# Kernel optimization log

Hardware: AMD Instinct MI355X
Metric: run time of the kernel (lower is better)

## Reference

```python
import jax, jax.numpy as jnp
import numpy as np

HIDDEN = 2048
VOCAB = 32768
SEQ = 4608
N_CHUNKS = 9
CAP = 30.0
IGNORE = -100


def setup_inputs() -> dict:
    key = jax.random.key(0)
    k1, k2, k3 = jax.random.split(key, 3)
    weight = (jax.random.normal(k1, (VOCAB, HIDDEN), dtype=jnp.float32) * 0.02).astype(jnp.bfloat16)
    hidden = jax.random.normal(k2, (1, SEQ, HIDDEN), dtype=jnp.float32)
    input_ids = jax.random.randint(k3, (1, SEQ), 0, VOCAB)
    attention_mask = jnp.ones((1, SEQ), dtype=jnp.int32)
    return {"weight": weight, "hidden": hidden, "input_ids": input_ids,
            "attention_mask": attention_mask}


def _build_labels(input_ids, attention_mask):
    # labels[t] = input_ids[t+1], masked-out positions and the final position -> -100
    ids = input_ids[0]
    am = attention_mask[0]
    lab = jnp.where(am[1:] == 0, IGNORE, ids[1:])            # [S-1]
    lab = jnp.concatenate([lab, jnp.full((1,), IGNORE, lab.dtype)])  # [S]
    return lab


def reference(weight, hidden, input_ids, attention_mask):
    labels = _build_labels(input_ids, attention_mask)        # [S]
    x = hidden.reshape(-1, HIDDEN)                           # [S, H] fp32
    chunk = SEQ // N_CHUNKS
    xs = x.reshape(N_CHUNKS, chunk, HIDDEN)
    ls = labels.reshape(N_CHUNKS, chunk)

    wT = weight.T                                            # [H, V] bf16

    def chunk_loss(args):
        xc, lc = args                                        # [c,H], [c]
        # softcapped logits: CAP * tanh((x @ W^T) / CAP), mm in bf16
        t = jnp.tanh((xc.astype(jnp.bfloat16) @ wT) / CAP).astype(jnp.float32)  # [c,V]
        z = CAP * (t - jnp.max(t, axis=1, keepdims=True))    # stable shifted logits
        logp = z - jnp.log(jnp.sum(jnp.exp(z), axis=1, keepdims=True))
        valid = lc != IGNORE
        idx = jnp.where(valid, lc, 0)
        nll = -jnp.take_along_axis(logp, idx[:, None], axis=1)[:, 0]
        return jnp.sum(jnp.where(valid, nll, 0.0))

    losses = jax.lax.map(chunk_loss, (xs, ls))               # [N_CHUNKS]
    return jnp.sum(losses)
```

## Files before the change

### kernel.cpp

```cpp
#include <hip/hip_runtime.h>
#include <hip/hip_bf16.h>
#include <cstdint>

#define S_LEN   4608
#define HID     2048
#define VOCAB_N 32768
#define CAPV    30.0f
#define IGNORE_IDX (-100)
#define NT512   512

typedef short bf16x8 __attribute__((ext_vector_type(8)));
typedef float f32x4  __attribute__((ext_vector_type(4)));

__device__ __forceinline__ unsigned short f2bf_rtne(float f) {
    unsigned int u = __float_as_uint(f);
    unsigned int r = u + 0x7fffu + ((u >> 16) & 1u);
    return (unsigned short)(r >> 16);
}
__device__ __forceinline__ float bfr(float f) {
    unsigned int u = __float_as_uint(f);
    unsigned int r = u + 0x7fffu + ((u >> 16) & 1u);
    return __uint_as_float(r & 0xffff0000u);
}
__device__ __forceinline__ float bf_lo(unsigned int u) { return __uint_as_float(u << 16); }
__device__ __forceinline__ float bf_hi(unsigned int u) { return __uint_as_float(u & 0xffff0000u); }
__device__ __forceinline__ float bfdot2(unsigned int x, unsigned int w) {
    return bf_lo(x) * bf_lo(w) + bf_hi(x) * bf_hi(w);
}
__device__ __forceinline__ float softcap_ref(float logit) {
    float lb = bfr(logit);
    float x  = bfr(lb / CAPV);
    float e  = __expf(2.0f * x);
    float t  = bfr((e - 1.0f) / (e + 1.0f));
    return CAPV * t;
}

__global__ void cvt_kernel(const float* __restrict__ h, unsigned short* __restrict__ xb,
                           float* __restrict__ out) {
    if (blockIdx.x == 0 && threadIdx.x == 0) out[0] = 0.0f;
    int i = blockIdx.x * blockDim.x + threadIdx.x;
    float4 v = ((const float4*)h)[i];
    ushort4 o;
    o.x = f2bf_rtne(v.x); o.y = f2bf_rtne(v.y);
    o.z = f2bf_rtne(v.z); o.w = f2bf_rtne(v.w);
    ((ushort4*)xb)[i] = o;
}

__global__ void gemm_lse_kernel(const unsigned short* __restrict__ X,
                                const unsigned short* __restrict__ W,
                                float* __restrict__ partL) {
    __shared__ __align__(16) unsigned short As[128 * 32];
    __shared__ __align__(16) unsigned short Bs[128 * 32];

    const int tid  = threadIdx.x;
    const int wave = tid >> 6;
    const int lane = tid & 63;
    const int tileM = blockIdx.x * 128;
    const int tileN = blockIdx.y * 128;

    const int lr = lane >> 2;
    const int cg = (lane & 3) ^ ((lane >> 4) & 3);

    const unsigned short* Abase = X + (size_t)(tileM + wave * 32) * HID + cg * 8;
    const unsigned short* Bbase = W + (size_t)(tileN + wave * 32) * HID + cg * 8;

    const int wr  = wave >> 1, wc = wave & 1;
    const int q   = lane >> 4, l16 = lane & 15;

    const int swz = (q ^ (l16 >> 2)) * 8;
    int arow[4], brow[4];
    #pragma unroll
    for (int t = 0; t < 4; ++t) {
        arow[t] = (wr * 64 + t * 16 + l16) * 32 + swz;
        brow[t] = (wc * 64 + t * 16 + l16) * 32 + swz;
    }

    f32x4 acc[4][4] = {};

    for (int k0 = 0; k0 < HID; k0 += 32) {
        __syncthreads();
        #pragma unroll
        for (int j = 0; j < 2; ++j) {
            const unsigned short* ga = Abase + (size_t)(j * 16 + lr) * HID + k0;
            __builtin_amdgcn_global_load_lds(
                (const __attribute__((address_space(1))) void*)ga,
                (__attribute__((address_space(3))) void*)&As[(wave * 32 + j * 16) * 32],
                16, 0, 0);
            const unsigned short* gb = Bbase + (size_t)(j * 16 + lr) * HID + k0;
            __builtin_amdgcn_global_load_lds(
                (const __attribute__((address_space(1))) void*)gb,
                (__attribute__((address_space(3))) void*)&Bs[(wave * 32 + j * 16) * 32],
                16, 0, 0);
        }
        __syncthreads();

        bf16x8 av[4], bv[4];
        #pragma unroll
        for (int t = 0; t < 4; ++t) {
            av[t] = *(const bf16x8*)&As[arow[t]];
            bv[t] = *(const bf16x8*)&Bs[brow[t]];
        }
        #pragma unroll
        for (int ti = 0; ti < 4; ++ti)
            #pragma unroll
            for (int tj = 0; tj < 4; ++tj)
                acc[ti][tj] = __builtin_amdgcn_mfma_f32_16x16x32_bf16(
                    av[ti], bv[tj], acc[ti][tj], 0, 0, 0);
    }

    const int rowbase = tileM + wr * 64;
    const int ntile   = blockIdx.y * 2 + wc;
    #pragma unroll
    for (int ti = 0; ti < 4; ++ti) {
        #pragma unroll
        for (int r = 0; r < 4; ++r) {
            float s = 0.0f;
            #pragma unroll
            for (int tj = 0; tj < 4; ++tj)
                s += __expf(softcap_ref(acc[ti][tj][r]));
            s += __shfl_xor(s, 1);
            s += __shfl_xor(s, 2);
            s += __shfl_xor(s, 4);
            s += __shfl_xor(s, 8);
            if (l16 == 0)
                partL[(size_t)(rowbase + ti * 16 + q * 4 + r) * NT512 + ntile] = s;
        }
    }
}

__global__ void row_reduce_kernel(const unsigned short* __restrict__ X,
                                  const unsigned short* __restrict__ W,
                                  const int* __restrict__ ids,
                                  const int* __restrict__ am,
                                  const float* __restrict__ partL,
                                  float* __restrict__ out) {
    __shared__ float blk[4];
    const int wave = threadIdx.x >> 6;
    const int lane = threadIdx.x & 63;
    const int r = blockIdx.x * 4 + wave;

    int lab = IGNORE_IDX;
    if (r < S_LEN - 1 && am[r + 1] != 0) lab = ids[r + 1];
    const bool valid = (lab >= 0 && lab < VOCAB_N);

    float dot = 0.0f;
    if (valid) {
        const unsigned short* xr = X + (size_t)r   * HID;
        const unsigned short* wr = W + (size_t)lab * HID;
        #pragma unroll
        for (int c = 0; c < 4; ++c) {
            const int off = c * 512 + lane * 8;
            uint4 xu = *(const uint4*)(xr + off);
            uint4 wu = *(const uint4*)(wr + off);
            dot += bfdot2(xu.x, wu.x) + bfdot2(xu.y, wu.y) +
                   bfdot2(xu.z, wu.z) + bfdot2(xu.w, wu.w);
        }
    }
    #pragma unroll
    for (int m = 1; m < 64; m <<= 1) dot += __shfl_xor(dot, m);

    float L = 0.0f;
    const float* pr = partL + (size_t)r * NT512;
    #pragma unroll
    for (int i = 0; i < 8; ++i) L += pr[i * 64 + lane];
    #pragma unroll
    for (int m = 1; m < 64; m <<= 1) L += __shfl_xor(L, m);

    if (lane == 0) {
        float loss = 0.0f;
        if (valid) loss = logf(L) - softcap_ref(dot);
        blk[wave] = loss;
    }
    __syncthreads();
    if (threadIdx.x == 0)
        atomicAdd(out, blk[0] + blk[1] + blk[2] + blk[3]);
}

extern "C" void kernel_launch(void* const* d_in, const int* in_sizes, int n_in,
                              void* d_out, int out_size, void* d_ws, size_t ws_size,
                              hipStream_t stream) {
    const unsigned short* W  = (const unsigned short*)d_in[0];
    const float*  hidden     = (const float*)d_in[1];
    const int*    ids        = (const int*)d_in[2];
    const int*    am         = (const int*)d_in[3];
    float* out = (float*)d_out;

    char* ws = (char*)d_ws;
    unsigned short* Xb = (unsigned short*)ws;
    float* partL       = (float*)(ws + (size_t)S_LEN * HID * 2);

    cvt_kernel<<<(S_LEN * HID / 4) / 256, 256, 0, stream>>>(hidden, Xb, out);

    dim3 g(S_LEN / 128, VOCAB_N / 128);
    gemm_lse_kernel<<<g, 256, 0, stream>>>(Xb, W, partL);

    row_reduce_kernel<<<S_LEN / 4, 256, 0, stream>>>(Xb, W, ids, am, partL, out);
}
```

Baseline: 1.019 ms.

## Use 256x256 tiles with double-buffered LDS and interleaved load/MFMA schedule

Rewrites the GEMM+LSE kernel to use 256x256 output tiles, 512 threads (8 waves) and a 64-wide K step. Global-to-LDS copies are double-buffered and interleaved with MFMA quarters under barriers and s_setprio, so memory latency overlaps compute. The larger tile raises arithmetic intensity and cuts the number of barriers per FLOP, at the cost of 128KB of LDS, heavy register use and a complex hand-written schedule.

```diff
diff --git a/kernel.cpp b/kernel.cpp
--- a/kernel.cpp
+++ b/kernel.cpp
@@ -8,6 +8,7 @@
 #define CAPV    30.0f
 #define IGNORE_IDX (-100)
 #define NT512   512
+#define NKT     32
 
 typedef short bf16x8 __attribute__((ext_vector_type(8)));
 typedef float f32x4  __attribute__((ext_vector_type(4)));
@@ -46,86 +47,155 @@
     ((ushort4*)xb)[i] = o;
 }
 
-__global__ void gemm_lse_kernel(const unsigned short* __restrict__ X,
-                                const unsigned short* __restrict__ W,
-                                float* __restrict__ partL) {
-    __shared__ __align__(16) unsigned short As[128 * 32];
-    __shared__ __align__(16) unsigned short Bs[128 * 32];
+__global__ __launch_bounds__(512, 2)
+void gemm_lse_kernel(const unsigned short* __restrict__ X,
+                     const unsigned short* __restrict__ W,
+                     float* __restrict__ partL) {
+    __shared__ __align__(16) unsigned short As[2][256 * 64];
+    __shared__ __align__(16) unsigned short Bs[2][256 * 64];
 
     const int tid  = threadIdx.x;
-    const int wave = tid >> 6;
+    const int wid  = tid >> 6;
     const int lane = tid & 63;
-    const int tileM = blockIdx.x * 128;
-    const int tileN = blockIdx.y * 128;
-
-    const int lr = lane >> 2;
-    const int cg = (lane & 3) ^ ((lane >> 4) & 3);
-
-    const unsigned short* Abase = X + (size_t)(tileM + wave * 32) * HID + cg * 8;
-    const unsigned short* Bbase = W + (size_t)(tileN + wave * 32) * HID + cg * 8;
-
-    const int wr  = wave >> 1, wc = wave & 1;
-    const int q   = lane >> 4, l16 = lane & 15;
-
-    const int swz = (q ^ (l16 >> 2)) * 8;
-    int arow[4], brow[4];
-    #pragma unroll
-    for (int t = 0; t < 4; ++t) {
-        arow[t] = (wr * 64 + t * 16 + l16) * 32 + swz;
-        brow[t] = (wc * 64 + t * 16 + l16) * 32 + swz;
-    }
-
-    f32x4 acc[4][4] = {};
-
-    for (int k0 = 0; k0 < HID; k0 += 32) {
-        __syncthreads();
-        #pragma unroll
-        for (int j = 0; j < 2; ++j) {
-            const unsigned short* ga = Abase + (size_t)(j * 16 + lr) * HID + k0;
-            __builtin_amdgcn_global_load_lds(
-                (const __attribute__((address_space(1))) void*)ga,
-                (__attribute__((address_space(3))) void*)&As[(wave * 32 + j * 16) * 32],
-                16, 0, 0);
-            const unsigned short* gb = Bbase + (size_t)(j * 16 + lr) * HID + k0;
-            __builtin_amdgcn_global_load_lds(
-                (const __attribute__((address_space(1))) void*)gb,
-                (__attribute__((address_space(3))) void*)&Bs[(wave * 32 + j * 16) * 32],
-                16, 0, 0);
-        }
-        __syncthreads();
-
-        bf16x8 av[4], bv[4];
-        #pragma unroll
-        for (int t = 0; t < 4; ++t) {
-            av[t] = *(const bf16x8*)&As[arow[t]];
-            bv[t] = *(const bf16x8*)&Bs[brow[t]];
-        }
-        #pragma unroll
-        for (int ti = 0; ti < 4; ++ti)
-            #pragma unroll
-            for (int tj = 0; tj < 4; ++tj)
-                acc[ti][tj] = __builtin_amdgcn_mfma_f32_16x16x32_bf16(
-                    av[ti], bv[tj], acc[ti][tj], 0, 0, 0);
-    }
-
-    const int rowbase = tileM + wr * 64;
-    const int ntile   = blockIdx.y * 2 + wc;
-    #pragma unroll
-    for (int ti = 0; ti < 4; ++ti) {
+    const int wr   = wid >> 2;
+    const int wc   = wid & 3;
+    const int q    = lane >> 4, l16 = lane & 15;
+    const int tileM = blockIdx.x * 256;
+    const int tileN = blockIdx.y * 256;
+
+    const int srow = lane >> 3;
+    const int csrc = (lane & 7) ^ srow;
+    const unsigned short* Ag = X + (size_t)(tileM + wid * 8 + srow) * HID + csrc * 8;
+    const unsigned short* Wg = W + (size_t)(tileN + wid * 8 + srow) * HID + csrc * 8;
+
+    const int abase = (wr * 128 + l16) * 64;
+    const int bbase = (wc * 64  + l16) * 64;
+    const int koff0 = ((q    ) ^ (l16 & 7)) * 8;
+    const int koff1 = ((q + 4) ^ (l16 & 7)) * 8;
+
+    bf16x8 av[8][2], bv[4][2];
+    f32x4  acc[8][4] = {};
+
+#define STAGE_A(BUF, H, KT) do {                                                          \
+    const unsigned short* _g = Ag + (size_t)(H) * 128 * HID + (size_t)(KT) * 64;          \
+    __builtin_amdgcn_global_load_lds(                                                     \
+        (const __attribute__((address_space(1))) void*)_g,                                \
+        (__attribute__((address_space(3))) void*)&As[BUF][((H) * 128 + wid * 8) * 64],    \
+        16, 0, 0);                                                                        \
+    __builtin_amdgcn_global_load_lds(                                                     \
+        (const __attribute__((address_space(1))) void*)(_g + (size_t)64 * HID),           \
+        (__attribute__((address_space(3))) void*)&As[BUF][((H) * 128 + 64 + wid * 8) * 64],\
+        16, 0, 0);                                                                        \
+} while (0)
+
+#define STAGE_B(BUF, H, KT) do {                                                          \
+    const unsigned short* _g = Wg + (size_t)(H) * 128 * HID + (size_t)(KT) * 64;          \
+    __builtin_amdgcn_global_load_lds(                                                     \
+        (const __attribute__((address_space(1))) void*)_g,                                \
+        (__attribute__((address_space(3))) void*)&Bs[BUF][((H) * 128 + wid * 8) * 64],    \
+        16, 0, 0);                                                                        \
+    __builtin_amdgcn_global_load_lds(                                                     \
+        (const __attribute__((address_space(1))) void*)(_g + (size_t)64 * HID),           \
+        (__attribute__((address_space(3))) void*)&Bs[BUF][((H) * 128 + 64 + wid * 8) * 64],\
+        16, 0, 0);                                                                        \
+} while (0)
+
+#define LDA(BUF, MH) do {                                                                 \
+    _Pragma("unroll") for (int fm = 0; fm < 4; ++fm) {                                    \
+        av[(MH) * 4 + fm][0] = *(const bf16x8*)&As[BUF][abase + ((MH) * 64 + fm * 16) * 64 + koff0]; \
+        av[(MH) * 4 + fm][1] = *(const bf16x8*)&As[BUF][abase + ((MH) * 64 + fm * 16) * 64 + koff1]; \
+    } } while (0)
+
+#define LDB(BUF, NH) do {                                                                 \
+    _Pragma("unroll") for (int fn = 0; fn < 2; ++fn) {                                    \
+        bv[(NH) * 2 + fn][0] = *(const bf16x8*)&Bs[BUF][bbase + ((NH) * 32 + fn * 16) * 64 + koff0]; \
+        bv[(NH) * 2 + fn][1] = *(const bf16x8*)&Bs[BUF][bbase + ((NH) * 32 + fn * 16) * 64 + koff1]; \
+    } } while (0)
+
+#define MFMAQ(MH, NH) do {                                                                \
+    _Pragma("unroll") for (int kk = 0; kk < 2; ++kk)                                      \
+    _Pragma("unroll") for (int fm = 0; fm < 4; ++fm)                                      \
+    _Pragma("unroll") for (int fn = 0; fn < 2; ++fn)                                      \
+        acc[(MH) * 4 + fm][(NH) * 2 + fn] = __builtin_amdgcn_mfma_f32_16x16x32_bf16(      \
+            av[(MH) * 4 + fm][kk], bv[(NH) * 2 + fn][kk],                                 \
+            acc[(MH) * 4 + fm][(NH) * 2 + fn], 0, 0, 0);                                  \
+} while (0)
+
+#define BAR()   __builtin_amdgcn_s_barrier()
+#define PRIO1() __builtin_amdgcn_s_setprio(1)
+#define PRIO0() __builtin_amdgcn_s_setprio(0)
+#define VMCNT4() asm volatile("s_waitcnt vmcnt(4)" ::: "memory")
+#define VMCNT0() asm volatile("s_waitcnt vmcnt(0)" ::: "memory")
+
+#define KTILE(CUR, NXT, T) do {                                                           \
+    LDA(CUR, 0); LDB(CUR, 0); STAGE_B(NXT, 0, (T) + 1);                                   \
+    BAR(); PRIO1(); MFMAQ(0, 0); PRIO0(); BAR();                                          \
+    LDA(CUR, 1); LDB(CUR, 1); STAGE_B(NXT, 1, (T) + 1);                                   \
+    BAR(); PRIO1(); MFMAQ(0, 1); PRIO0(); BAR();                                          \
+    STAGE_A(CUR, 0, (T) + 2);                                                             \
+    BAR(); PRIO1(); MFMAQ(1, 0); PRIO0(); BAR();                                          \
+    STAGE_A(CUR, 1, (T) + 2);                                                             \
+    BAR(); PRIO1(); MFMAQ(1, 1); PRIO0();                                                 \
+    VMCNT4(); BAR();                                                                      \
+} while (0)
+
+    STAGE_A(0, 0, 0); STAGE_A(0, 1, 0);
+    STAGE_B(0, 0, 0); STAGE_B(0, 1, 0);
+    STAGE_A(1, 0, 1); STAGE_A(1, 1, 1);
+    VMCNT4();
+    BAR();
+
+    #pragma unroll 1
+    for (int t = 0; t < NKT - 2; t += 2) {
+        KTILE(0, 1, t);
+        KTILE(1, 0, t + 1);
+    }
+
+    LDA(0, 0); LDB(0, 0); STAGE_B(1, 0, 31);
+    BAR(); PRIO1(); MFMAQ(0, 0); PRIO0(); BAR();
+    LDA(0, 1); LDB(0, 1); STAGE_B(1, 1, 31);
+    BAR(); PRIO1(); MFMAQ(0, 1); PRIO0(); BAR();
+    BAR(); PRIO1(); MFMAQ(1, 0); PRIO0(); BAR();
+    PRIO1(); MFMAQ(1, 1); PRIO0();
+    VMCNT0(); BAR();
+
+    LDA(1, 0); LDB(1, 0);
+    PRIO1(); MFMAQ(0, 0); PRIO0();
+    LDA(1, 1); LDB(1, 1);
+    PRIO1(); MFMAQ(0, 1); PRIO0();
+    PRIO1(); MFMAQ(1, 0); PRIO0();
+    PRIO1(); MFMAQ(1, 1); PRIO0();
+
+    const int rowbase = tileM + wr * 128;
+    const int ntile   = blockIdx.y * 4 + wc;
+    #pragma unroll
+    for (int m = 0; m < 8; ++m) {
         #pragma unroll
         for (int r = 0; r < 4; ++r) {
             float s = 0.0f;
             #pragma unroll
-            for (int tj = 0; tj < 4; ++tj)
-                s += __expf(softcap_ref(acc[ti][tj][r]));
+            for (int n = 0; n < 4; ++n)
+                s += __expf(softcap_ref(acc[m][n][r]));
             s += __shfl_xor(s, 1);
             s += __shfl_xor(s, 2);
             s += __shfl_xor(s, 4);
             s += __shfl_xor(s, 8);
             if (l16 == 0)
-                partL[(size_t)(rowbase + ti * 16 + q * 4 + r) * NT512 + ntile] = s;
+                partL[(size_t)(rowbase + m * 16 + q * 4 + r) * NT512 + ntile] = s;
         }
     }
+
+#undef STAGE_A
+#undef STAGE_B
+#undef LDA
+#undef LDB
+#undef MFMAQ
+#undef BAR
+#undef PRIO1
+#undef PRIO0
+#undef VMCNT4
+#undef VMCNT0
+#undef KTILE
 }
 
 __global__ void row_reduce_kernel(const unsigned short* __restrict__ X,
@@ -191,8 +261,8 @@
 
     cvt_kernel<<<(S_LEN * HID / 4) / 256, 256, 0, stream>>>(hidden, Xb, out);
 
-    dim3 g(S_LEN / 128, VOCAB_N / 128);
-    gemm_lse_kernel<<<g, 256, 0, stream>>>(Xb, W, partL);
+    dim3 g(S_LEN / 256, VOCAB_N / 256);
+    gemm_lse_kernel<<<g, 512, 0, stream>>>(Xb, W, partL);
 
     row_reduce_kernel<<<S_LEN / 4, 256, 0, stream>>>(Xb, W, ids, am, partL, out);
 }
```

Measured after the change: 1.091 ms. 1.07x slower.

## Enlarge GEMM tile to 256x256 with 16 waves and double-buffered LDS

Applied to the files above, without the earlier changes.

Moves the fused GEMM+LSE kernel from 128x128 tiles with 4 waves to 256x256 tiles with 16 waves per block. Each wave still computes a 64x64 sub-tile. The K loop now double-buffers the A/B LDS tiles so the next k-slice is loaded while MFMAs run on the current one. The aim is to raise operand reuse per global load and hide load latency. The costs are more LDS per block (64KB), fewer blocks in the grid (18x128), and a launch_bounds request of 4 blocks per CU that may not fit.

```diff
diff --git a/kernel.cpp b/kernel.cpp
--- a/kernel.cpp
+++ b/kernel.cpp
@@ -8,6 +8,7 @@
 #define CAPV    30.0f
 #define IGNORE_IDX (-100)
 #define NT512   512
+#define NKS     64
 
 typedef short bf16x8 __attribute__((ext_vector_type(8)));
 typedef float f32x4  __attribute__((ext_vector_type(4)));
@@ -46,86 +47,92 @@
     ((ushort4*)xb)[i] = o;
 }
 
-__global__ void gemm_lse_kernel(const unsigned short* __restrict__ X,
-                                const unsigned short* __restrict__ W,
-                                float* __restrict__ partL) {
-    __shared__ __align__(16) unsigned short As[128 * 32];
-    __shared__ __align__(16) unsigned short Bs[128 * 32];
+__global__ __launch_bounds__(1024, 4)
+void gemm_lse_kernel(const unsigned short* __restrict__ X,
+                     const unsigned short* __restrict__ W,
+                     float* __restrict__ partL) {
+    __shared__ __align__(16) unsigned short As[2][256 * 32];
+    __shared__ __align__(16) unsigned short Bs[2][256 * 32];
 
     const int tid  = threadIdx.x;
-    const int wave = tid >> 6;
+    const int wid  = tid >> 6;
     const int lane = tid & 63;
-    const int tileM = blockIdx.x * 128;
-    const int tileN = blockIdx.y * 128;
+    const int wr   = wid >> 2;
+    const int wc   = wid & 3;
+    const int q    = lane >> 4, l16 = lane & 15;
+    const int tileM = blockIdx.x * 256;
+    const int tileN = blockIdx.y * 256;
 
     const int lr = lane >> 2;
     const int cg = (lane & 3) ^ ((lane >> 4) & 3);
-
-    const unsigned short* Abase = X + (size_t)(tileM + wave * 32) * HID + cg * 8;
-    const unsigned short* Bbase = W + (size_t)(tileN + wave * 32) * HID + cg * 8;
-
-    const int wr  = wave >> 1, wc = wave & 1;
-    const int q   = lane >> 4, l16 = lane & 15;
-
-    const int swz = (q ^ (l16 >> 2)) * 8;
-    int arow[4], brow[4];
-    #pragma unroll
-    for (int t = 0; t < 4; ++t) {
-        arow[t] = (wr * 64 + t * 16 + l16) * 32 + swz;
-        brow[t] = (wc * 64 + t * 16 + l16) * 32 + swz;
-    }
+    const unsigned short* Ag = X + (size_t)(tileM + wid * 16 + lr) * HID + cg * 8;
+    const unsigned short* Wg = W + (size_t)(tileN + wid * 16 + lr) * HID + cg * 8;
+
+    const int swz   = (q ^ (l16 >> 2)) * 8;
+    const int abase = (wr * 64 + l16) * 32 + swz;
+    const int bbase = (wc * 64 + l16) * 32 + swz;
 
     f32x4 acc[4][4] = {};
 
-    for (int k0 = 0; k0 < HID; k0 += 32) {
+#define STAGE(BUF, T) do {                                                                \
+    __builtin_amdgcn_global_load_lds(                                                     \
+        (const __attribute__((address_space(1))) void*)(Ag + (size_t)(T) * 32),           \
+        (__attribute__((address_space(3))) void*)&As[BUF][wid * 512], 16, 0, 0);          \
+    __builtin_amdgcn_global_load_lds(                                                     \
+        (const __attribute__((address_space(1))) void*)(Wg + (size_t)(T) * 32),           \
+        (__attribute__((address_space(3))) void*)&Bs[BUF][wid * 512], 16, 0, 0);          \
+} while (0)
+
+#define COMPUTE(BUF) do {                                                                 \
+    bf16x8 av[4], bv[4];                                                                  \
+    _Pragma("unroll") for (int f = 0; f < 4; ++f) {                                       \
+        av[f] = *(const bf16x8*)&As[BUF][abase + f * 512];                                \
+        bv[f] = *(const bf16x8*)&Bs[BUF][bbase + f * 512];                                \
+    }                                                                                     \
+    _Pragma("unroll") for (int m = 0; m < 4; ++m)                                         \
+    _Pragma("unroll") for (int n = 0; n < 4; ++n)                                         \
+        acc[m][n] = __builtin_amdgcn_mfma_f32_16x16x32_bf16(av[m], bv[n],                 \
+                                                            acc[m][n], 0, 0, 0);          \
+} while (0)
+
+    STAGE(0, 0);
+
+    #pragma unroll 1
+    for (int t = 0; t < NKS - 2; t += 2) {
         __syncthreads();
-        #pragma unroll
-        for (int j = 0; j < 2; ++j) {
-            const unsigned short* ga = Abase + (size_t)(j * 16 + lr) * HID + k0;
-            __builtin_amdgcn_global_load_lds(
-                (const __attribute__((address_space(1))) void*)ga,
-                (__attribute__((address_space(3))) void*)&As[(wave * 32 + j * 16) * 32],
-                16, 0, 0);
-            const unsigned short* gb = Bbase + (size_t)(j * 16 + lr) * HID + k0;
-            __builtin_amdgcn_global_load_lds(
-                (const __attribute__((address_space(1))) void*)gb,
-                (__attribute__((address_space(3))) void*)&Bs[(wave * 32 + j * 16) * 32],
-                16, 0, 0);
-        }
+        STAGE(1, t + 1);
+        COMPUTE(0);
         __syncthreads();
-
-        bf16x8 av[4], bv[4];
-        #pragma unroll
-        for (int t = 0; t < 4; ++t) {
-            av[t] = *(const bf16x8*)&As[arow[t]];
-            bv[t] = *(const bf16x8*)&Bs[brow[t]];
-        }
-        #pragma unroll
-        for (int ti = 0; ti < 4; ++ti)
-            #pragma unroll
-            for (int tj = 0; tj < 4; ++tj)
-                acc[ti][tj] = __builtin_amdgcn_mfma_f32_16x16x32_bf16(
-                    av[ti], bv[tj], acc[ti][tj], 0, 0, 0);
-    }
+        STAGE(0, t + 2);
+        COMPUTE(1);
+    }
+    __syncthreads();
+    STAGE(1, NKS - 1);
+    COMPUTE(0);
+    __syncthreads();
+    COMPUTE(1);
 
     const int rowbase = tileM + wr * 64;
-    const int ntile   = blockIdx.y * 2 + wc;
-    #pragma unroll
-    for (int ti = 0; ti < 4; ++ti) {
+    const int ntile   = blockIdx.y * 4 + wc;
+    #pragma unroll
+    for (int m = 0; m < 4; ++m) {
         #pragma unroll
         for (int r = 0; r < 4; ++r) {
             float s = 0.0f;
             #pragma unroll
-            for (int tj = 0; tj < 4; ++tj)
-                s += __expf(softcap_ref(acc[ti][tj][r]));
+            for (int n = 0; n < 4; ++n)
+                s += __expf(softcap_ref(acc[m][n][r]));
             s += __shfl_xor(s, 1);
             s += __shfl_xor(s, 2);
             s += __shfl_xor(s, 4);
             s += __shfl_xor(s, 8);
             if (l16 == 0)
-                partL[(size_t)(rowbase + ti * 16 + q * 4 + r) * NT512 + ntile] = s;
+                partL[(size_t)(rowbase + m * 16 + q * 4 + r) * NT512 + ntile] = s;
         }
     }
+
+#undef STAGE
+#undef COMPUTE
 }
 
 __global__ void row_reduce_kernel(const unsigned short* __restrict__ X,
@@ -191,8 +198,8 @@
 
     cvt_kernel<<<(S_LEN * HID / 4) / 256, 256, 0, stream>>>(hidden, Xb, out);
 
-    dim3 g(S_LEN / 128, VOCAB_N / 128);
-    gemm_lse_kernel<<<g, 256, 0, stream>>>(Xb, W, partL);
+    dim3 g(S_LEN / 256, VOCAB_N / 256);
+    gemm_lse_kernel<<<g, 1024, 0, stream>>>(Xb, W, partL);
 
     row_reduce_kernel<<<S_LEN / 4, 256, 0, stream>>>(Xb, W, ids, am, partL, out);
 }
```

Measured after the change: 1.121 ms. +10.0%, slower.
